# Performance work log

Measured on AMD Instinct MI355X. Metric: run time of the kernel, lower is better.

Reference implementation:

```python
import jax, jax.numpy as jnp
import numpy as np

N_LAYERS = 4
D_MODEL = 256
N_HEADS = 8
D_FF = 2 * D_MODEL
EPS_ATTN = 1e-6
EPS_LN = 1e-5


def setup_inputs() -> dict:
    key = jax.random.key(0)
    ks = jax.random.split(key, 20)
    C, F, L = D_MODEL, D_FF, N_LAYERS
    s = 0.02
    return {
        "ref_feature": jax.random.normal(ks[0], (4, C, 128, 128), jnp.float32),
        # per-layer stacked params (torch nn.Linear convention: y = x @ W.T + b)
        "Wq": jax.random.normal(ks[1], (L, C, C), jnp.float32) * s,
        "bq": jnp.zeros((L, C), jnp.float32),
        "Wk": jax.random.normal(ks[2], (L, C, C), jnp.float32) * s,
        "bk": jnp.zeros((L, C), jnp.float32),
        "Wv": jax.random.normal(ks[3], (L, C, C), jnp.float32) * s,
        "bv": jnp.zeros((L, C), jnp.float32),
        "Wo": jax.random.normal(ks[4], (L, C, C), jnp.float32) * s,
        "bo": jnp.zeros((L, C), jnp.float32),
        "g1": jnp.ones((L, C), jnp.float32),
        "be1": jnp.zeros((L, C), jnp.float32),
        "W1": jax.random.normal(ks[5], (L, F, C), jnp.float32) * s,
        "c1": jnp.zeros((L, F), jnp.float32),
        "W2": jax.random.normal(ks[6], (L, C, F), jnp.float32) * s,
        "c2": jnp.zeros((L, C), jnp.float32),
        "g2": jnp.ones((L, C), jnp.float32),
        "be2": jnp.zeros((L, C), jnp.float32),
    }


def _layer_norm(x, g, b):
    m = jnp.mean(x, axis=-1, keepdims=True)
    v = jnp.mean(jnp.square(x - m), axis=-1, keepdims=True)
    return (x - m) * jax.lax.rsqrt(v + EPS_LN) * g + b


def _feature_map(x):
    return jax.nn.elu(x) + 1.0


def reference(ref_feature, Wq, bq, Wk, bk, Wv, bv, Wo, bo,
              g1, be1, W1, c1, W2, c2, g2, be2):
    N, C, H, W = ref_feature.shape
    Hh, D = N_HEADS, C // N_HEADS
    # patch embed: flatten to tokens [N, HW, C]
    x = ref_feature.reshape(N, C, H * W).transpose(0, 2, 1)

    def body(x, p):
        (Wq_, bq_, Wk_, bk_, Wv_, bv_, Wo_, bo_,
         g1_, be1_, W1_, c1_, W2_, c2_, g2_, be2_) = p
        L = x.shape[1]
        q = (x @ Wq_.T + bq_).reshape(N, L, Hh, D)
        k = (x @ Wk_.T + bk_).reshape(N, L, Hh, D)
        v = (x @ Wv_.T + bv_).reshape(N, L, Hh, D)
        Q = _feature_map(q)
        K = _feature_map(k)
        KV = jnp.einsum('nshd,nshm->nhmd', K, v)            # [N,H,D,D]
        Z = 1.0 / (jnp.einsum('nlhd,nhd->nlh', Q, K.sum(axis=1)) + EPS_ATTN)
        attn = jnp.einsum('nlhd,nhmd,nlh->nlhm', Q, KV, Z).reshape(N, L, C)
        x = _layer_norm(x + attn @ Wo_.T + bo_, g1_, be1_)
        y = jax.nn.relu(x @ W1_.T + c1_) @ W2_.T + c2_
        x = _layer_norm(x + y, g2_, be2_)
        return x, x

    params = (Wq, bq, Wk, bk, Wv, bv, Wo, bo,
              g1, be1, W1, c1, W2, c2, g2, be2)
    _, ys = jax.lax.scan(body, x, params)
    # ys: [n_layers, N, HW, C] -> [n_layers, N, C, H, W]
    return ys.transpose(0, 1, 3, 2).reshape(N_LAYERS, N, C, H, W)
```

## Files before the change

kernel.cpp:

```cpp
#include <hip/hip_runtime.h>
#include <hip/hip_bf16.h>
#include <math.h>

#define NB     4
#define CDIM   256
#define HWDIM  16384
#define LTOK   16384
#define NH     8
#define HD     32
#define FF     512
#define MTOK   (NB * LTOK)
#define NLAYER 4

typedef __bf16 bf16x8 __attribute__((ext_vector_type(8)));
typedef __bf16 bf16x4 __attribute__((ext_vector_type(4)));
typedef float  floatx4 __attribute__((ext_vector_type(4)));

#define GLD16(gp, lp)                                                        \
    __builtin_amdgcn_global_load_lds(                                        \
        (const __attribute__((address_space(1))) void*)(gp),                 \
        (__attribute__((address_space(3))) void*)(lp), 16, 0, 0)

__global__ __launch_bounds__(256)
void f2b_kernel(const float* __restrict__ in, __bf16* __restrict__ out)
{
    int i = (blockIdx.x * 256 + threadIdx.x) * 4;
    float4 f = *(const float4*)&in[i];
    bf16x4 h;
    h[0] = (__bf16)f.x; h[1] = (__bf16)f.y; h[2] = (__bf16)f.z; h[3] = (__bf16)f.w;
    *(bf16x4*)&out[i] = h;
}

__global__ __launch_bounds__(256)
void patch_embed(const float* __restrict__ in, __bf16* __restrict__ out)
{
    __shared__ float tile[32][33];
    const int n = blockIdx.z;
    const int hw0 = blockIdx.x * 32, c0 = blockIdx.y * 32;
    const int tx = threadIdx.x, ty = threadIdx.y;
#pragma unroll
    for (int i = 0; i < 32; i += 8)
        tile[ty + i][tx] = in[(long long)n * CDIM * HWDIM + (long long)(c0 + ty + i) * HWDIM + hw0 + tx];
    __syncthreads();
#pragma unroll
    for (int i = 0; i < 32; i += 8)
        out[(long long)(n * HWDIM + hw0 + ty + i) * CDIM + c0 + tx] = (__bf16)tile[tx][ty + i];
}

__global__ __launch_bounds__(256)
void out_transpose(const __bf16* __restrict__ X, float* __restrict__ out)
{
    __shared__ float tile[32][33];
    const int n = blockIdx.z;
    const int c0 = blockIdx.x * 32, l0 = blockIdx.y * 32;
    const int tid = threadIdx.x;
    {
        int row = tid >> 3, cq = tid & 7;
        bf16x4 x4 = *(const bf16x4*)&X[(long long)(n * LTOK + l0 + row) * CDIM + c0 + cq * 4];
#pragma unroll
        for (int j = 0; j < 4; ++j)
            tile[row][cq * 4 + j] = (float)x4[j];
    }
    __syncthreads();
    {
        int r = tid >> 3, lg = tid & 7;
        float4 o;
        o.x = tile[lg * 4 + 0][r];
        o.y = tile[lg * 4 + 1][r];
        o.z = tile[lg * 4 + 2][r];
        o.w = tile[lg * 4 + 3][r];
        *(float4*)&out[(long long)n * CDIM * LTOK + (long long)(c0 + r) * LTOK + l0 + lg * 4] = o;
    }
}

#define WIDE_PROLOGUE()                                                      \
    const int tid  = threadIdx.x;                                            \
    const int lane = tid & 63;                                               \
    const int wave = tid >> 6;                                               \
    const int m0   = blockIdx.x * 128;                                       \
    const int l15  = lane & 15;                                              \
    const int quad = lane >> 4;                                              \
    const int wm   = (wave & 1) * 64;                                        \
    const int wn   = (wave >> 1) * 128;                                      \
    floatx4 acc[4][8];                                                       \
    _Pragma("unroll")                                                        \
    for (int i = 0; i < 4; ++i)                                              \
        _Pragma("unroll")                                                    \
        for (int j = 0; j < 8; ++j)                                          \
            acc[i][j] = (floatx4){0.f, 0.f, 0.f, 0.f};

#define WIDE_STAGE(Aq, Bq, KD)                                               \
    __syncthreads();                                                         \
    _Pragma("unroll")                                                        \
    for (int i = 0; i < 4; ++i) {                                            \
        int s = wave * 256 + i * 64 + lane;                                  \
        int row = s >> 3, kq = s & 7;                                        \
        GLD16(&(Aq)[(long long)(m0 + row) * (KD) + k0 + kq * 8],             \
              &Asl[(wave * 256 + i * 64) * 8]);                              \
    }                                                                        \
    _Pragma("unroll")                                                        \
    for (int i = 0; i < 8; ++i) {                                            \
        int s = wave * 512 + i * 64 + lane;                                  \
        int row = s >> 3, kq = s & 7;                                        \
        GLD16(&(Bq)[(long long)row * (KD) + k0 + kq * 8],                    \
              &Bsl[(wave * 512 + i * 64) * 8]);                              \
    }                                                                        \
    __syncthreads();

#define WIDE_MFMA()                                                          \
    _Pragma("unroll")                                                        \
    for (int ko = 0; ko < 2; ++ko) {                                         \
        bf16x8 af[4], bfr[8];                                                \
        _Pragma("unroll")                                                    \
        for (int mt = 0; mt < 4; ++mt)                                       \
            af[mt] = *(const bf16x8*)&Asl[(wm + mt * 16 + l15) * 64 + ko * 32 + quad * 8]; \
        _Pragma("unroll")                                                    \
        for (int nt = 0; nt < 8; ++nt)                                       \
            bfr[nt] = *(const bf16x8*)&Bsl[(wn + nt * 16 + l15) * 64 + ko * 32 + quad * 8]; \
        _Pragma("unroll")                                                    \
        for (int mt = 0; mt < 4; ++mt)                                       \
            _Pragma("unroll")                                                \
            for (int nt = 0; nt < 8; ++nt)                                   \
                acc[mt][nt] = __builtin_amdgcn_mfma_f32_16x16x32_bf16(       \
                    bfr[nt], af[mt], acc[mt][nt], 0, 0, 0);                  \
    }

__device__ __forceinline__ int t_idx(int c, int s)
{
    return c * 64 + (s ^ ((c & 7) << 3));
}

__global__ __launch_bounds__(256, 2)
void qkv_kv(const __bf16* __restrict__ X,
            const __bf16* __restrict__ Wq, const __bf16* __restrict__ Wk,
            const __bf16* __restrict__ Wv,
            const float* __restrict__ bq, const float* __restrict__ bk,
            const float* __restrict__ bv,
            __bf16* __restrict__ Qo, float* __restrict__ pKV,
            float* __restrict__ pKS)
{
    __shared__ __bf16 Asl[64 * 256];
    __shared__ __bf16 Bsl[256 * 64];
    const int tid  = threadIdx.x;
    const int lane = tid & 63;
    const int wave = tid >> 6;
    const int m0   = blockIdx.x * 64;
    const int l15  = lane & 15;
    const int quad = lane >> 4;
    const int wm   = (wave & 1) * 32;
    const int wn   = (wave >> 1) * 128;

#pragma unroll
    for (int i = 0; i < 8; ++i) {
        int s = i * 256 + wave * 64 + lane;
        int row = s >> 5, kq = s & 31;
        GLD16(&X[(long long)(m0 + row) * CDIM + kq * 8], &Asl[(i * 256 + wave * 64) * 8]);
    }

    floatx4 acc[2][8];
    bf16x4  kbf[2][8];

#pragma unroll
    for (int sel = 0; sel < 3; ++sel) {
        const __bf16* B = (sel == 0) ? Wq : (sel == 1) ? Wk : Wv;
#pragma unroll
        for (int i = 0; i < 2; ++i)
#pragma unroll
            for (int j = 0; j < 8; ++j)
                acc[i][j] = (floatx4){0.f, 0.f, 0.f, 0.f};

        for (int k0 = 0; k0 < CDIM; k0 += 64) {
            __syncthreads();
#pragma unroll
            for (int i = 0; i < 8; ++i) {
                int s = wave * 512 + i * 64 + lane;
                int row = s >> 3, kq = s & 7;
                GLD16(&B[(long long)row * CDIM + k0 + kq * 8], &Bsl[(wave * 512 + i * 64) * 8]);
            }
            __syncthreads();
#pragma unroll
            for (int ko = 0; ko < 2; ++ko) {
                bf16x8 af[2], bfr[8];
#pragma unroll
                for (int mt = 0; mt < 2; ++mt)
                    af[mt] = *(const bf16x8*)&Asl[(wm + mt * 16 + l15) * 256 + k0 + ko * 32 + quad * 8];
#pragma unroll
                for (int nt = 0; nt < 8; ++nt)
                    bfr[nt] = *(const bf16x8*)&Bsl[(wn + nt * 16 + l15) * 64 + ko * 32 + quad * 8];
#pragma unroll
                for (int mt = 0; mt < 2; ++mt)
#pragma unroll
                    for (int nt = 0; nt < 8; ++nt)
                        acc[mt][nt] = __builtin_amdgcn_mfma_f32_16x16x32_bf16(
                            bfr[nt], af[mt], acc[mt][nt], 0, 0, 0);
            }
        }

        if (sel == 0) {
#pragma unroll
            for (int mt = 0; mt < 2; ++mt) {
                int row = m0 + wm + mt * 16 + l15;
#pragma unroll
                for (int nt = 0; nt < 8; ++nt) {
                    int col0 = wn + nt * 16 + quad * 4;
                    float4 bb = *(const float4*)&bq[col0];
                    bf16x4 o;
#pragma unroll
                    for (int r = 0; r < 4; ++r) {
                        float v = acc[mt][nt][r] + ((r == 0) ? bb.x : (r == 1) ? bb.y : (r == 2) ? bb.z : bb.w);
                        v = v > 0.f ? v + 1.f : __expf(v);
                        o[r] = (__bf16)v;
                    }
                    *(bf16x4*)&Qo[(long long)row * CDIM + col0] = o;
                }
            }
        } else if (sel == 1) {
#pragma unroll
            for (int mt = 0; mt < 2; ++mt)
#pragma unroll
                for (int nt = 0; nt < 8; ++nt) {
                    int col0 = wn + nt * 16 + quad * 4;
                    float4 bb = *(const float4*)&bk[col0];
#pragma unroll
                    for (int r = 0; r < 4; ++r) {
                        float v = acc[mt][nt][r] + ((r == 0) ? bb.x : (r == 1) ? bb.y : (r == 2) ? bb.z : bb.w);
                        v = v > 0.f ? v + 1.f : __expf(v);
                        kbf[mt][nt][r] = (__bf16)v;
                    }
                }
        }
    }

    __syncthreads();
    {
        __bf16* KT = Bsl;
        __bf16* VT = Asl;
#pragma unroll
        for (int nt = 0; nt < 8; ++nt) {
            int col0 = wn + nt * 16 + quad * 4;
            float4 bb = *(const float4*)&bv[col0];
#pragma unroll
            for (int mt = 0; mt < 2; ++mt) {
                int row_t = wm + mt * 16 + l15;
#pragma unroll
                for (int r = 0; r < 4; ++r) {
                    KT[t_idx(col0 + r, row_t)] = kbf[mt][nt][r];
                    float vv = acc[mt][nt][r] + ((r == 0) ? bb.x : (r == 1) ? bb.y : (r == 2) ? bb.z : bb.w);
                    VT[t_idx(col0 + r, row_t)] = (__bf16)vv;
                }
            }
        }
    }
    __syncthreads();

    {
        const __bf16* KT = Bsl;
        float s = 0.f;
#pragma unroll 8
        for (int i = 0; i < 64; ++i) {
            int ss = (i + tid) & 63;
            s += (float)KT[t_idx(tid, ss)];
        }
        pKS[(long long)blockIdx.x * 256 + tid] = s;
    }

    {
        const __bf16* KT = Bsl;
        const __bf16* VT = Asl;
        float* outKV = pKV + (long long)blockIdx.x * 8192;
#pragma unroll
        for (int hh = 0; hh < 2; ++hh) {
            int h = wave * 2 + hh;
            floatx4 kv[2][2];
#pragma unroll
            for (int mi = 0; mi < 2; ++mi)
#pragma unroll
                for (int di = 0; di < 2; ++di)
                    kv[mi][di] = (floatx4){0.f, 0.f, 0.f, 0.f};
#pragma unroll
            for (int ks = 0; ks < 2; ++ks) {
                bf16x8 a[2], b[2];
#pragma unroll
                for (int mi = 0; mi < 2; ++mi)
                    a[mi] = *(const bf16x8*)&VT[t_idx(h * 32 + mi * 16 + l15, ks * 32 + quad * 8)];
#pragma unroll
                for (int di = 0; di < 2; ++di)
                    b[di] = *(const bf16x8*)&KT[t_idx(h * 32 + di * 16 + l15, ks * 32 + quad * 8)];
#pragma unroll
                for (int mi = 0; mi < 2; ++mi)
#pragma unroll
                    for (int di = 0; di < 2; ++di)
                        kv[mi][di] = __builtin_amdgcn_mfma_f32_16x16x32_bf16(
                            a[mi], b[di], kv[mi][di], 0, 0, 0);
            }
#pragma unroll
            for (int mi = 0; mi < 2; ++mi)
#pragma unroll
                for (int di = 0; di < 2; ++di)
#pragma unroll
                    for (int r = 0; r < 4; ++r)
                        outKV[(long long)h * 1024 + (mi * 16 + quad * 4 + r) * 32 + di * 16 + l15]
                            = kv[mi][di][r];
        }
    }
}

__global__ __launch_bounds__(256)
void kv_reduce(const float* __restrict__ pKV, const float* __restrict__ pKS,
               float* __restrict__ KV, float* __restrict__ KS)
{
    __shared__ float red[256];
    const int bid = blockIdx.x, tid = threadIdx.x;
    if (bid < 256) {
        int o = bid * 128 + (tid & 127);
        int half = tid >> 7;
        int n = o >> 13, r = o & 8191;
        const float* p = pKV + ((long long)n * 256 + half * 128) * 8192 + r;
        float s = 0.f;
#pragma unroll 8
        for (int b = 0; b < 128; ++b) s += p[(long long)b * 8192];
        red[tid] = s;
        __syncthreads();
        if (half == 0) KV[o] = red[tid] + red[tid + 128];
    } else {
        int n = bid - 256;
        const float* p = pKS + (long long)n * 256 * 256 + tid;
        float s = 0.f;
#pragma unroll 8
        for (int b = 0; b < 256; ++b) s += p[b * 256];
        KS[n * 256 + tid] = s;
    }
}

__global__ __launch_bounds__(256, 2)
void gemm_relu(const __bf16* __restrict__ A, const __bf16* __restrict__ Bw,
               const float* __restrict__ bias, __bf16* __restrict__ C)
{
    __shared__ __bf16 Asl[128 * 64];
    __shared__ __bf16 Bsl[256 * 64];
    const int n_base = blockIdx.y * 256;
    const __bf16* B = Bw + (long long)n_base * CDIM;

    WIDE_PROLOGUE()
    for (int k0 = 0; k0 < CDIM; k0 += 64) {
        WIDE_STAGE(A, B, CDIM)
        WIDE_MFMA()
    }
#pragma unroll
    for (int mt = 0; mt < 4; ++mt) {
        int row = m0 + wm + mt * 16 + l15;
#pragma unroll
        for (int nt = 0; nt < 8; ++nt) {
            int col0 = wn + nt * 16 + quad * 4;
            float4 bb = *(const float4*)&bias[n_base + col0];
            bf16x4 o;
#pragma unroll
            for (int r = 0; r < 4; ++r) {
                float v = acc[mt][nt][r] + ((r == 0) ? bb.x : (r == 1) ? bb.y : (r == 2) ? bb.z : bb.w);
                o[r] = (__bf16)(v > 0.f ? v : 0.f);
            }
            *(bf16x4*)&C[(long long)row * FF + n_base + col0] = o;
        }
    }
}

template <int KDIM>
__global__ __launch_bounds__(256, 2)
void gemm_ln(const __bf16* __restrict__ A, const __bf16* __restrict__ B,
             const float* __restrict__ bias, __bf16* X,
             const float* __restrict__ g, const float* __restrict__ be)
{
    __shared__ __bf16 Asl[128 * 64];
    __shared__ __bf16 Bsl[256 * 64];

    WIDE_PROLOGUE()
    for (int k0 = 0; k0 < KDIM; k0 += 64) {
        WIDE_STAGE(A, B, KDIM)
        WIDE_MFMA()
    }

#pragma unroll
    for (int mt = 0; mt < 4; ++mt) {
        int row = m0 + wm + mt * 16 + l15;
#pragma unroll
        for (int nt = 0; nt < 8; ++nt) {
            int col0 = wn + nt * 16 + quad * 4;
            float4 bb = *(const float4*)&bias[col0];
            bf16x4 xr = *(const bf16x4*)&X[(long long)row * CDIM + col0];
            acc[mt][nt][0] += bb.x + (float)xr[0];
            acc[mt][nt][1] += bb.y + (float)xr[1];
            acc[mt][nt][2] += bb.z + (float)xr[2];
            acc[mt][nt][3] += bb.w + (float)xr[3];
        }
    }

    float psum[4], psq[4];
#pragma unroll
    for (int mt = 0; mt < 4; ++mt) {
        float s = 0.f, q = 0.f;
#pragma unroll
        for (int nt = 0; nt < 8; ++nt)
#pragma unroll
            for (int r = 0; r < 4; ++r) {
                float v = acc[mt][nt][r];
                s += v; q += v * v;
            }
        s += __shfl_xor(s, 16, 64); s += __shfl_xor(s, 32, 64);
        q += __shfl_xor(q, 16, 64); q += __shfl_xor(q, 32, 64);
        psum[mt] = s; psq[mt] = q;
    }

    float* red = (float*)Asl;
    const int half = wave >> 1;
    __syncthreads();
    if (quad == 0) {
#pragma unroll
        for (int mt = 0; mt < 4; ++mt) {
            int rl = wm + mt * 16 + l15;
            red[rl * 4 + half * 2 + 0] = psum[mt];
            red[rl * 4 + half * 2 + 1] = psq[mt];
        }
    }
    __syncthreads();

#pragma unroll
    for (int mt = 0; mt < 4; ++mt) {
        int rl  = wm + mt * 16 + l15;
        float tot = red[rl * 4 + 0] + red[rl * 4 + 2];
        float tsq = red[rl * 4 + 1] + red[rl * 4 + 3];
        float mean = tot * (1.f / 256.f);
        float var  = tsq * (1.f / 256.f) - mean * mean;
        float rstd = rsqrtf(var + 1e-5f);
        int row = m0 + rl;
#pragma unroll
        for (int nt = 0; nt < 8; ++nt) {
            int col0 = wn + nt * 16 + quad * 4;
            float4 gg = *(const float4*)&g[col0];
            float4 ee = *(const float4*)&be[col0];
            bf16x4 o;
            o[0] = (__bf16)((acc[mt][nt][0] - mean) * rstd * gg.x + ee.x);
            o[1] = (__bf16)((acc[mt][nt][1] - mean) * rstd * gg.y + ee.y);
            o[2] = (__bf16)((acc[mt][nt][2] - mean) * rstd * gg.z + ee.z);
            o[3] = (__bf16)((acc[mt][nt][3] - mean) * rstd * gg.w + ee.w);
            *(bf16x4*)&X[(long long)row * CDIM + col0] = o;
        }
    }
}

__global__ __launch_bounds__(256)
void attn_kernel(const __bf16* __restrict__ Q, const float* __restrict__ KV,
                 const float* __restrict__ KS, __bf16* __restrict__ out)
{
    __shared__ float q_lds[16 * 256];
    const int n = blockIdx.y;
    const int tid = threadIdx.x;
    const int h = tid >> 5;
    const int m = tid & 31;

    float4 kvr[8], ksr[8];
    {
        const float4* kvp = (const float4*)&KV[(((long long)n * NH + h) * HD + m) * HD];
        const float4* ksp = (const float4*)&KS[((long long)n * NH + h) * HD];
#pragma unroll
        for (int i = 0; i < 8; ++i) { kvr[i] = kvp[i]; ksr[i] = ksp[i]; }
    }

    for (int it = 0; it < 4; ++it) {
        int l0 = blockIdx.x * 64 + it * 16;
        __syncthreads();
#pragma unroll
        for (int i = 0; i < 4; ++i) {
            int e = tid * 4 + i * 1024;
            int row = e >> 8, col = e & 255;
            bf16x4 q4 = *(const bf16x4*)&Q[(long long)(n * LTOK + l0 + row) * CDIM + col];
            float4 f;
            f.x = (float)q4[0]; f.y = (float)q4[1]; f.z = (float)q4[2]; f.w = (float)q4[3];
            *(float4*)&q_lds[e] = f;
        }
        __syncthreads();
#pragma unroll 2
        for (int t = 0; t < 16; ++t) {
            const float4* qr = (const float4*)&q_lds[t * 256 + h * 32];
            float num = 0.f, den = 0.f;
#pragma unroll
            for (int i = 0; i < 8; ++i) {
                float4 q4 = qr[i];
                num += q4.x * kvr[i].x + q4.y * kvr[i].y + q4.z * kvr[i].z + q4.w * kvr[i].w;
                den += q4.x * ksr[i].x + q4.y * ksr[i].y + q4.z * ksr[i].z + q4.w * ksr[i].w;
            }
            out[(long long)(n * LTOK + l0 + t) * CDIM + tid] = (__bf16)(num / (den + 1e-6f));
        }
    }
}

extern "C" void kernel_launch(void* const* d_in, const int* in_sizes, int n_in,
                              void* d_out, int out_size, void* d_ws, size_t ws_size,
                              hipStream_t stream)
{
    const float* ref = (const float*)d_in[0];
    const float* Wq  = (const float*)d_in[1];  const float* bq = (const float*)d_in[2];
    const float* Wk  = (const float*)d_in[3];  const float* bk = (const float*)d_in[4];
    const float* Wv  = (const float*)d_in[5];  const float* bv = (const float*)d_in[6];
    const float* Wo  = (const float*)d_in[7];  const float* bo = (const float*)d_in[8];
    const float* g1  = (const float*)d_in[9];  const float* be1 = (const float*)d_in[10];
    const float* W1  = (const float*)d_in[11]; const float* c1 = (const float*)d_in[12];
    const float* W2  = (const float*)d_in[13]; const float* c2 = (const float*)d_in[14];
    const float* g2  = (const float*)d_in[15]; const float* be2 = (const float*)d_in[16];
    float* out = (float*)d_out;

    const size_t SZ = (size_t)MTOK * CDIM;
    __bf16* Xb = (__bf16*)d_ws;
    __bf16* Qb = Xb + SZ;
    __bf16* Kb = Qb + SZ;
    __bf16* Vb = Kb + SZ;
    __bf16* Hb = Vb + SZ;
    float*  KVb = (float*)(Hb + 2 * SZ);
    float*  KSb = KVb + NB * NH * HD * HD;
    __bf16* Wqb = (__bf16*)(KSb + NB * NH * HD);
    const size_t WC = (size_t)NLAYER * CDIM * CDIM;
    const size_t WF = (size_t)NLAYER * FF * CDIM;
    __bf16* Wkb = Wqb + WC;
    __bf16* Wvb = Wkb + WC;
    __bf16* Wob = Wvb + WC;
    __bf16* W1b = Wob + WC;
    __bf16* W2b = W1b + WF;

    f2b_kernel<<<WC / 1024, 256, 0, stream>>>(Wq, Wqb);
    f2b_kernel<<<WC / 1024, 256, 0, stream>>>(Wk, Wkb);
    f2b_kernel<<<WC / 1024, 256, 0, stream>>>(Wv, Wvb);
    f2b_kernel<<<WC / 1024, 256, 0, stream>>>(Wo, Wob);
    f2b_kernel<<<WF / 1024, 256, 0, stream>>>(W1, W1b);
    f2b_kernel<<<WF / 1024, 256, 0, stream>>>(W2, W2b);

    dim3 tb(32, 8);
    patch_embed<<<dim3(HWDIM / 32, CDIM / 32, NB), tb, 0, stream>>>(ref, Xb);

    for (int l = 0; l < NLAYER; ++l) {
        const __bf16* Wq_l = Wqb + (size_t)l * CDIM * CDIM;
        const __bf16* Wk_l = Wkb + (size_t)l * CDIM * CDIM;
        const __bf16* Wv_l = Wvb + (size_t)l * CDIM * CDIM;
        const __bf16* Wo_l = Wob + (size_t)l * CDIM * CDIM;
        const __bf16* W1_l = W1b + (size_t)l * FF * CDIM;
        const __bf16* W2_l = W2b + (size_t)l * CDIM * FF;
        const float* bq_l = bq + (size_t)l * CDIM;
        const float* bk_l = bk + (size_t)l * CDIM;
        const float* bv_l = bv + (size_t)l * CDIM;
        const float* bo_l = bo + (size_t)l * CDIM;
        const float* c1_l = c1 + (size_t)l * FF;
        const float* c2_l = c2 + (size_t)l * CDIM;
        const float* g1_l = g1 + (size_t)l * CDIM;
        const float* g2_l = g2 + (size_t)l * CDIM;
        const float* be1_l = be1 + (size_t)l * CDIM;
        const float* be2_l = be2 + (size_t)l * CDIM;

        qkv_kv<<<MTOK / 64, 256, 0, stream>>>(
            Xb, Wq_l, Wk_l, Wv_l, bq_l, bk_l, bv_l,
            Qb, (float*)Kb, (float*)Vb);

        kv_reduce<<<260, 256, 0, stream>>>((const float*)Kb, (const float*)Vb, KVb, KSb);

        attn_kernel<<<dim3(LTOK / 64, NB), 256, 0, stream>>>(Qb, KVb, KSb, Kb);

        gemm_ln<CDIM><<<MTOK / 128, 256, 0, stream>>>(Kb, Wo_l, bo_l, Xb, g1_l, be1_l);

        gemm_relu<<<dim3(MTOK / 128, 2), 256, 0, stream>>>(Xb, W1_l, c1_l, Hb);

        gemm_ln<FF><<<MTOK / 128, 256, 0, stream>>>(Hb, W2_l, c2_l, Xb, g2_l, be2_l);

        out_transpose<<<dim3(CDIM / 32, LTOK / 32, NB), 256, 0, stream>>>(
            Xb, out + (size_t)l * NB * CDIM * LTOK);
    }
}
```

Baseline: 1.398 ms.

## Fuse FFN up/down GEMMs, LayerNorm and output transpose into one kernel

```diff
diff --git a/kernel.cpp b/kernel.cpp
--- a/kernel.cpp
+++ b/kernel.cpp
@@ -45,32 +45,6 @@
 #pragma unroll
     for (int i = 0; i < 32; i += 8)
         out[(long long)(n * HWDIM + hw0 + ty + i) * CDIM + c0 + tx] = (__bf16)tile[tx][ty + i];
-}
-
-__global__ __launch_bounds__(256)
-void out_transpose(const __bf16* __restrict__ X, float* __restrict__ out)
-{
-    __shared__ float tile[32][33];
-    const int n = blockIdx.z;
-    const int c0 = blockIdx.x * 32, l0 = blockIdx.y * 32;
-    const int tid = threadIdx.x;
-    {
-        int row = tid >> 3, cq = tid & 7;
-        bf16x4 x4 = *(const bf16x4*)&X[(long long)(n * LTOK + l0 + row) * CDIM + c0 + cq * 4];
-#pragma unroll
-        for (int j = 0; j < 4; ++j)
-            tile[row][cq * 4 + j] = (float)x4[j];
-    }
-    __syncthreads();
-    {
-        int r = tid >> 3, lg = tid & 7;
-        float4 o;
-        o.x = tile[lg * 4 + 0][r];
-        o.y = tile[lg * 4 + 1][r];
-        o.z = tile[lg * 4 + 2][r];
-        o.w = tile[lg * 4 + 3][r];
-        *(float4*)&out[(long long)n * CDIM * LTOK + (long long)(c0 + r) * LTOK + l0 + lg * 4] = o;
-    }
 }
 
 #define WIDE_PROLOGUE()                                                      \
@@ -332,38 +306,6 @@
     }
 }
 
-__global__ __launch_bounds__(256, 2)
-void gemm_relu(const __bf16* __restrict__ A, const __bf16* __restrict__ Bw,
-               const float* __restrict__ bias, __bf16* __restrict__ C)
-{
-    __shared__ __bf16 Asl[128 * 64];
-    __shared__ __bf16 Bsl[256 * 64];
-    const int n_base = blockIdx.y * 256;
-    const __bf16* B = Bw + (long long)n_base * CDIM;
-
-    WIDE_PROLOGUE()
-    for (int k0 = 0; k0 < CDIM; k0 += 64) {
-        WIDE_STAGE(A, B, CDIM)
-        WIDE_MFMA()
-    }
-#pragma unroll
-    for (int mt = 0; mt < 4; ++mt) {
-        int row = m0 + wm + mt * 16 + l15;
-#pragma unroll
-        for (int nt = 0; nt < 8; ++nt) {
-            int col0 = wn + nt * 16 + quad * 4;
-            float4 bb = *(const float4*)&bias[n_base + col0];
-            bf16x4 o;
-#pragma unroll
-            for (int r = 0; r < 4; ++r) {
-                float v = acc[mt][nt][r] + ((r == 0) ? bb.x : (r == 1) ? bb.y : (r == 2) ? bb.z : bb.w);
-                o[r] = (__bf16)(v > 0.f ? v : 0.f);
-            }
-            *(bf16x4*)&C[(long long)row * FF + n_base + col0] = o;
-        }
-    }
-}
-
 template <int KDIM>
 __global__ __launch_bounds__(256, 2)
 void gemm_ln(const __bf16* __restrict__ A, const __bf16* __restrict__ B,
@@ -444,6 +386,170 @@
             o[3] = (__bf16)((acc[mt][nt][3] - mean) * rstd * gg.w + ee.w);
             *(bf16x4*)&X[(long long)row * CDIM + col0] = o;
         }
+    }
+}
+
+__global__ __launch_bounds__(512, 2)
+void ffn_fused(__bf16* __restrict__ X,
+               const __bf16* __restrict__ W1, const float* __restrict__ c1,
+               const __bf16* __restrict__ W2, const float* __restrict__ c2,
+               const float* __restrict__ g,  const float* __restrict__ be,
+               float* __restrict__ out)
+{
+    __shared__ __bf16 Asl[64 * 256];
+    __shared__ __bf16 Bsl[256 * 64];
+    __shared__ __bf16 Hs[64 * 512];
+
+    const int tid  = threadIdx.x;
+    const int lane = tid & 63;
+    const int wave = tid >> 6;
+    const int m0   = blockIdx.x * 64;
+    const int l15  = lane & 15;
+    const int quad = lane >> 4;
+    const int wr   = (wave & 3) * 16;
+    const int wc   = (wave >> 2) * 128;
+    const int row  = wr + l15;
+    const int rx   = row & 7;
+
+#pragma unroll
+    for (int i = 0; i < 4; ++i) {
+        int s = i * 512 + wave * 64 + lane;
+        int rr = s >> 5, c8 = s & 31;
+        GLD16(&X[(long long)(m0 + rr) * CDIM + c8 * 8], &Asl[s * 8]);
+    }
+
+    floatx4 acc[8];
+
+#pragma unroll
+    for (int p = 0; p < 2; ++p) {
+#pragma unroll
+        for (int j = 0; j < 8; ++j) acc[j] = (floatx4){0.f, 0.f, 0.f, 0.f};
+        for (int k0 = 0; k0 < CDIM; k0 += 64) {
+            __syncthreads();
+#pragma unroll
+            for (int i = 0; i < 4; ++i) {
+                int s = i * 512 + wave * 64 + lane;
+                int rr = s >> 3, kq = s & 7;
+                GLD16(&W1[(long long)(p * 256 + rr) * CDIM + k0 + kq * 8], &Bsl[s * 8]);
+            }
+            __syncthreads();
+#pragma unroll
+            for (int ko = 0; ko < 2; ++ko) {
+                bf16x8 af = *(const bf16x8*)&Asl[row * 256 + k0 + ko * 32 + quad * 8];
+                bf16x8 bfr[8];
+#pragma unroll
+                for (int nt = 0; nt < 8; ++nt)
+                    bfr[nt] = *(const bf16x8*)&Bsl[(wc + nt * 16 + l15) * 64 + ko * 32 + quad * 8];
+#pragma unroll
+                for (int nt = 0; nt < 8; ++nt)
+                    acc[nt] = __builtin_amdgcn_mfma_f32_16x16x32_bf16(bfr[nt], af, acc[nt], 0, 0, 0);
+            }
+        }
+#pragma unroll
+        for (int nt = 0; nt < 8; ++nt) {
+            int hc = p * 256 + wc + nt * 16 + quad * 4;
+            float4 bb = *(const float4*)&c1[hc];
+            bf16x4 o;
+#pragma unroll
+            for (int r = 0; r < 4; ++r) {
+                float v = acc[nt][r] + ((r == 0) ? bb.x : (r == 1) ? bb.y : (r == 2) ? bb.z : bb.w);
+                o[r] = (__bf16)(v > 0.f ? v : 0.f);
+            }
+            int hc8 = hc >> 3;
+            *(bf16x4*)&Hs[row * 512 + (((hc8 ^ rx) << 3) | (hc & 7))] = o;
+        }
+    }
+
+#pragma unroll
+    for (int j = 0; j < 8; ++j) acc[j] = (floatx4){0.f, 0.f, 0.f, 0.f};
+    for (int k0 = 0; k0 < FF; k0 += 64) {
+        __syncthreads();
+#pragma unroll
+        for (int i = 0; i < 4; ++i) {
+            int s = i * 512 + wave * 64 + lane;
+            int rr = s >> 3, kq = s & 7;
+            GLD16(&W2[(long long)rr * FF + k0 + kq * 8], &Bsl[s * 8]);
+        }
+        __syncthreads();
+#pragma unroll
+        for (int ko = 0; ko < 2; ++ko) {
+            int k8 = (k0 >> 3) + ko * 4 + quad;
+            bf16x8 af = *(const bf16x8*)&Hs[row * 512 + ((k8 ^ rx) << 3)];
+            bf16x8 bfr[8];
+#pragma unroll
+            for (int nt = 0; nt < 8; ++nt)
+                bfr[nt] = *(const bf16x8*)&Bsl[(wc + nt * 16 + l15) * 64 + ko * 32 + quad * 8];
+#pragma unroll
+            for (int nt = 0; nt < 8; ++nt)
+                acc[nt] = __builtin_amdgcn_mfma_f32_16x16x32_bf16(bfr[nt], af, acc[nt], 0, 0, 0);
+        }
+    }
+
+#pragma unroll
+    for (int nt = 0; nt < 8; ++nt) {
+        int col0 = wc + nt * 16 + quad * 4;
+        float4 bb = *(const float4*)&c2[col0];
+        bf16x4 xr = *(const bf16x4*)&Asl[row * 256 + col0];
+        acc[nt][0] += bb.x + (float)xr[0];
+        acc[nt][1] += bb.y + (float)xr[1];
+        acc[nt][2] += bb.z + (float)xr[2];
+        acc[nt][3] += bb.w + (float)xr[3];
+    }
+
+    float s = 0.f, q = 0.f;
+#pragma unroll
+    for (int nt = 0; nt < 8; ++nt)
+#pragma unroll
+        for (int r = 0; r < 4; ++r) {
+            float v = acc[nt][r];
+            s += v; q += v * v;
+        }
+    s += __shfl_xor(s, 16, 64); s += __shfl_xor(s, 32, 64);
+    q += __shfl_xor(q, 16, 64); q += __shfl_xor(q, 32, 64);
+
+    float* red = (float*)Bsl;
+    const int half = wave >> 2;
+    __syncthreads();
+    if (quad == 0) {
+        red[row * 4 + half * 2 + 0] = s;
+        red[row * 4 + half * 2 + 1] = q;
+    }
+    __syncthreads();
+
+    float tot  = red[row * 4 + 0] + red[row * 4 + 2];
+    float tsq  = red[row * 4 + 1] + red[row * 4 + 3];
+    float mean = tot * (1.f / 256.f);
+    float var  = tsq * (1.f / 256.f) - mean * mean;
+    float rstd = rsqrtf(var + 1e-5f);
+
+    float* Hf = (float*)Hs;
+#pragma unroll
+    for (int nt = 0; nt < 8; ++nt) {
+        int col0 = wc + nt * 16 + quad * 4;
+        float4 gg = *(const float4*)&g[col0];
+        float4 ee = *(const float4*)&be[col0];
+        bf16x4 o;
+#pragma unroll
+        for (int r = 0; r < 4; ++r) {
+            float gv = (r == 0) ? gg.x : (r == 1) ? gg.y : (r == 2) ? gg.z : gg.w;
+            float ev = (r == 0) ? ee.x : (r == 1) ? ee.y : (r == 2) ? ee.z : ee.w;
+            float v  = (acc[nt][r] - mean) * rstd * gv + ev;
+            o[r] = (__bf16)v;
+            Hf[(col0 + r) * 64 + row] = v;
+        }
+        *(bf16x4*)&X[(long long)(m0 + row) * CDIM + col0] = o;
+    }
+    __syncthreads();
+
+    {
+        const int n  = m0 >> 14;
+        const int l0 = m0 & (LTOK - 1);
+        int c  = tid >> 1;
+        int hh = (tid & 1) * 32;
+        const float4* src = (const float4*)&Hf[c * 64 + hh];
+        float4* dst = (float4*)&out[(long long)n * CDIM * LTOK + (long long)c * LTOK + l0 + hh];
+#pragma unroll
+        for (int i = 0; i < 8; ++i) dst[i] = src[i];
     }
 }
 
@@ -563,11 +669,8 @@
 
         gemm_ln<CDIM><<<MTOK / 128, 256, 0, stream>>>(Kb, Wo_l, bo_l, Xb, g1_l, be1_l);
 
-        gemm_relu<<<dim3(MTOK / 128, 2), 256, 0, stream>>>(Xb, W1_l, c1_l, Hb);
-
-        gemm_ln<FF><<<MTOK / 128, 256, 0, stream>>>(Hb, W2_l, c2_l, Xb, g2_l, be2_l);
-
-        out_transpose<<<dim3(CDIM / 32, LTOK / 32, NB), 256, 0, stream>>>(
-            Xb, out + (size_t)l * NB * CDIM * LTOK);
-    }
-}
+        ffn_fused<<<MTOK / 64, 512, 0, stream>>>(
+            Xb, W1_l, c1_l, W2_l, c2_l, g2_l, be2_l,
+            out + (size_t)l * NB * CDIM * LTOK);
+    }
+}
```

Result: slower. 1.594 ms (+14.0%).
